# Optimization experiments

Hardware: AMD Instinct MI355X
Metric: run time of the kernel (lower is better)

## Reference

```python
import jax, jax.numpy as jnp
import numpy as np

N, M, K = 131072, 32, 16
EPS64 = 2.220446049250313e-16  # np.finfo(np.float64).eps, as in the original


def setup_inputs() -> dict:
    key = jax.random.key(0)
    k1, k2, k3, k4, k5 = jax.random.split(key, 5)
    X = jax.random.normal(k1, (N, M), dtype=jnp.float32)
    Wk0 = jax.random.normal(k2, (K,), dtype=jnp.float32)
    W = jax.random.normal(k3, (M, K, K), dtype=jnp.float32)
    mu = jax.random.uniform(k4, (K, K), minval=-4.0, maxval=4.0, dtype=jnp.float32)
    sigma = 0.5 + 0.5 * jax.random.uniform(k5, (K, K), dtype=jnp.float32)
    return {"X": X, "Wk0": Wk0, "W": W, "mu": mu, "sigma": sigma}


def reference(X, Wk0, W, mu, sigma):
    # Softmax-normalized TT weights (original: softmax(Wk0), softmax(W, axis=1))
    z = jax.nn.softmax(Wk0)          # (K,)
    Wn = jax.nn.softmax(W, axis=1)   # (M, K, K)
    inv_norm = 1.0 / (sigma * jnp.sqrt(2.0 * jnp.pi))  # (K, K) Gaussian normalizer

    def step(v, inp):
        # v: (N, K) running left-product z @ resT_0 @ ... @ resT_{i-1}
        x_i, w_i = inp               # x_i: (N,), w_i: (K, K)
        d = (x_i[:, None, None] - mu) / sigma          # (N, K, K)
        B = jnp.exp(-0.5 * d * d) * inv_norm           # Normal(mu, sigma).prob(x)
        res = w_i[None, :, :] * B                      # res[n,a,b] == original res[a,b,n]
        # original: products = products @ res.T, so v_new[n,b] = sum_a v[n,a] * res[n,b,a]
        v_new = jnp.einsum('na,nba->nb', v, res)
        return v_new, None

    v0 = jnp.broadcast_to(z, (X.shape[0], z.shape[0]))   # z @ identity start
    v_final, _ = jax.lax.scan(step, v0, (X.T, Wn))       # scan over M steps
    likelihoods = jnp.sum(v_final, axis=1)               # sum(z @ products, axis=1)
    return jnp.log(likelihoods + EPS64)
```

## Files before the change

kernel.cpp:

```cpp
#include <hip/hip_runtime.h>
#include <cmath>


#define TT_N 131072
#define TT_M 32

typedef float v2f __attribute__((ext_vector_type(2)));
typedef float v4f __attribute__((ext_vector_type(4)));

#define WS_Z 0
#define WS_P 16
#define WS_Q (16 + 256)
#define WS_R (16 + 512)
#define TBL_FLOATS (512 + 8192)

__global__ __launch_bounds__(512) void tt_prep(const float* __restrict__ Wk0,
                                               const float* __restrict__ W,
                                               const float* __restrict__ mu,
                                               const float* __restrict__ sigma,
                                               float* __restrict__ ws) {
    const int t = threadIdx.x;
    const float LOG2E = 1.4426950408889634f;
    float* z  = ws + WS_Z;
    float* PP = ws + WS_P;
    float* QQ = ws + WS_Q;
    float* RT = ws + WS_R;

    if (t < 16) {
        float mx = -1e30f;
        for (int i = 0; i < 16; ++i) mx = fmaxf(mx, Wk0[i]);
        float se = 0.f;
        for (int i = 0; i < 16; ++i) se += __expf(Wk0[i] - mx);
        z[t] = __expf(Wk0[t] - mx) / se;
    }

    if (t < 256) {
        const int a = t >> 4, b = t & 15;
        float s  = sigma[b * 16 + a];
        float mm = mu[b * 16 + a];
        float c2 = 0.72134752044448f / (s * s);
        PP[a * 16 + b] = -c2;
        QQ[a * 16 + b] = 2.0f * c2 * mm;
    }

    const int m = t >> 4;
    const int a = t & 15;
    const float* Wc = W + m * 256 + a;
    float mx = -1e30f;
    #pragma unroll
    for (int b = 0; b < 16; ++b) mx = fmaxf(mx, Wc[b * 16]);
    float se = 0.f;
    #pragma unroll
    for (int b = 0; b < 16; ++b) se += __expf(Wc[b * 16] - mx);
    float lse = __log2f(se);
    #pragma unroll
    for (int b = 0; b < 16; ++b) {
        float s     = sigma[b * 16 + a];
        float mm    = mu[b * 16 + a];
        float inv_s = 1.0f / s;
        float c2    = 0.72134752044448f / (s * s);
        float lw    = (Wc[b * 16] - mx) * LOG2E - lse;
        RT[m * 256 + a * 16 + b] =
            lw + __log2f(inv_s * 0.3989422804014327f) - c2 * mm * mm;
    }
}

__global__ __launch_bounds__(256) void tt_main(const float* __restrict__ X,
                                               const float* __restrict__ ws,
                                               float* __restrict__ out) {
    __shared__ float lds[TBL_FLOATS];
    {
        const v4f* src = (const v4f*)(ws + WS_P);
        v4f* dst = (v4f*)lds;
        for (int i = threadIdx.x; i < TBL_FLOATS / 4; i += 256) dst[i] = src[i];
    }
    __syncthreads();

    const int n = blockIdx.x * 256 + threadIdx.x;
    const float* zp = ws + WS_Z;

    v2f v[8], acc[8];
    #pragma unroll
    for (int p = 0; p < 8; ++p) v[p] = (v2f){zp[2 * p], zp[2 * p + 1]};

    const float* xp = X + (size_t)n * TT_M;
    float S = 1.f;
    float xn = xp[0];

    #pragma unroll 1
    for (int m = 0; m < TT_M; ++m) {
        const float xm = xn;
        xn = xp[(m + 1 < TT_M) ? m + 1 : m];
        const float xq = xm * xm;
        const v2f xx  = {xm, xm};
        const v2f xx2 = {xq, xq};

        int lo = 0;
        asm volatile("" : "+v"(lo));
        const float* Pm = lds + lo;
        const float* Qm = lds + 256 + lo;
        const float* Rm = lds + 512 + m * 256;

        #pragma unroll
        for (int p = 0; p < 8; ++p) acc[p] = (v2f){0.f, 0.f};

        #pragma unroll
        for (int a = 0; a < 16; ++a) {
            const float vas = (a & 1) ? v[a >> 1].y : v[a >> 1].x;
            const v2f va2 = {vas, vas};
            #pragma unroll
            for (int h = 0; h < 4; ++h) {
                v4f P4 = *(const v4f*)(Pm + a * 16 + h * 4);
                v4f Q4 = *(const v4f*)(Qm + a * 16 + h * 4);
                v4f R4 = *(const v4f*)(Rm + a * 16 + h * 4);
                v2f t0 = __builtin_elementwise_fma(Q4.xy, xx, R4.xy);
                v2f s0 = __builtin_elementwise_fma(P4.xy, xx2, t0);
                v2f t1 = __builtin_elementwise_fma(Q4.zw, xx, R4.zw);
                v2f s1 = __builtin_elementwise_fma(P4.zw, xx2, t1);
                v2f e0, e1;
                e0.x = __builtin_amdgcn_exp2f(s0.x);
                e0.y = __builtin_amdgcn_exp2f(s0.y);
                e1.x = __builtin_amdgcn_exp2f(s1.x);
                e1.y = __builtin_amdgcn_exp2f(s1.y);
                acc[h * 2]     = __builtin_elementwise_fma(va2, e0, acc[h * 2]);
                acc[h * 2 + 1] = __builtin_elementwise_fma(va2, e1, acc[h * 2 + 1]);
            }
        }

        #pragma unroll
        for (int p = 0; p < 8; ++p) v[p] = acc[p];
        v2f u0 = (acc[0] + acc[1]) + (acc[2] + acc[3]);
        v2f u1 = (acc[4] + acc[5]) + (acc[6] + acc[7]);
        v2f u  = u0 + u1;
        S = u.x + u.y;
        if (__all(S < 5e-17f)) break;
    }

    out[n] = logf(S + 2.2204460492503131e-16f);
}

extern "C" void kernel_launch(void* const* d_in, const int* in_sizes, int n_in,
                              void* d_out, int out_size, void* d_ws, size_t ws_size,
                              hipStream_t stream) {
    const float* X     = (const float*)d_in[0];
    const float* Wk0   = (const float*)d_in[1];
    const float* W     = (const float*)d_in[2];
    const float* mu    = (const float*)d_in[3];
    const float* sigma = (const float*)d_in[4];
    float* out = (float*)d_out;
    float* ws  = (float*)d_ws;

    tt_prep<<<1, 512, 0, stream>>>(Wk0, W, mu, sigma, ws);
    tt_main<<<TT_N / 256, 256, 0, stream>>>(X, ws, out);
}
```

Baseline: 100.7 us.

## Split each sample's K-wide recurrence across four lanes with shuffle exchange

```diff
diff --git a/kernel.cpp b/kernel.cpp
--- a/kernel.cpp
+++ b/kernel.cpp
@@ -65,21 +65,31 @@
     }
 }
 
-__global__ __launch_bounds__(256) void tt_main(const float* __restrict__ X,
+static __device__ __forceinline__ v2f shfl_xor_v2f(v2f x, int mask) {
+    v2f r;
+    r.x = __shfl_xor(x.x, mask, 64);
+    r.y = __shfl_xor(x.y, mask, 64);
+    return r;
+}
+
+__global__ __launch_bounds__(512) void tt_main(const float* __restrict__ X,
                                                const float* __restrict__ ws,
                                                float* __restrict__ out) {
     __shared__ float lds[TBL_FLOATS];
     {
         const v4f* src = (const v4f*)(ws + WS_P);
         v4f* dst = (v4f*)lds;
-        for (int i = threadIdx.x; i < TBL_FLOATS / 4; i += 256) dst[i] = src[i];
+        for (int i = threadIdx.x; i < TBL_FLOATS / 4; i += 512) dst[i] = src[i];
     }
     __syncthreads();
 
-    const int n = blockIdx.x * 256 + threadIdx.x;
+    const int tid  = blockIdx.x * 512 + threadIdx.x;
+    const int n    = tid >> 2;
+    const int g    = tid & 3;
+    const int boff = g << 2;
+
     const float* zp = ws + WS_Z;
-
-    v2f v[8], acc[8];
+    v2f v[8];
     #pragma unroll
     for (int p = 0; p < 8; ++p) v[p] = (v2f){zp[2 * p], zp[2 * p + 1]};
 
@@ -101,42 +111,54 @@
         const float* Qm = lds + 256 + lo;
         const float* Rm = lds + 512 + m * 256;
 
-        #pragma unroll
-        for (int p = 0; p < 8; ++p) acc[p] = (v2f){0.f, 0.f};
+        v2f a0, a1;
 
         #pragma unroll
         for (int a = 0; a < 16; ++a) {
             const float vas = (a & 1) ? v[a >> 1].y : v[a >> 1].x;
             const v2f va2 = {vas, vas};
-            #pragma unroll
-            for (int h = 0; h < 4; ++h) {
-                v4f P4 = *(const v4f*)(Pm + a * 16 + h * 4);
-                v4f Q4 = *(const v4f*)(Qm + a * 16 + h * 4);
-                v4f R4 = *(const v4f*)(Rm + a * 16 + h * 4);
-                v2f t0 = __builtin_elementwise_fma(Q4.xy, xx, R4.xy);
-                v2f s0 = __builtin_elementwise_fma(P4.xy, xx2, t0);
-                v2f t1 = __builtin_elementwise_fma(Q4.zw, xx, R4.zw);
-                v2f s1 = __builtin_elementwise_fma(P4.zw, xx2, t1);
-                v2f e0, e1;
-                e0.x = __builtin_amdgcn_exp2f(s0.x);
-                e0.y = __builtin_amdgcn_exp2f(s0.y);
-                e1.x = __builtin_amdgcn_exp2f(s1.x);
-                e1.y = __builtin_amdgcn_exp2f(s1.y);
-                acc[h * 2]     = __builtin_elementwise_fma(va2, e0, acc[h * 2]);
-                acc[h * 2 + 1] = __builtin_elementwise_fma(va2, e1, acc[h * 2 + 1]);
+            const int base = a * 16 + boff;
+            v4f P4 = *(const v4f*)(Pm + base);
+            v4f Q4 = *(const v4f*)(Qm + base);
+            v4f R4 = *(const v4f*)(Rm + base);
+            v2f t0 = __builtin_elementwise_fma(Q4.xy, xx, R4.xy);
+            v2f s0 = __builtin_elementwise_fma(P4.xy, xx2, t0);
+            v2f t1 = __builtin_elementwise_fma(Q4.zw, xx, R4.zw);
+            v2f s1 = __builtin_elementwise_fma(P4.zw, xx2, t1);
+            v2f e0, e1;
+            e0.x = __builtin_amdgcn_exp2f(s0.x);
+            e0.y = __builtin_amdgcn_exp2f(s0.y);
+            e1.x = __builtin_amdgcn_exp2f(s1.x);
+            e1.y = __builtin_amdgcn_exp2f(s1.y);
+            if (a == 0) { a0 = va2 * e0; a1 = va2 * e1; }
+            else {
+                a0 = __builtin_elementwise_fma(va2, e0, a0);
+                a1 = __builtin_elementwise_fma(va2, e1, a1);
             }
         }
 
-        #pragma unroll
-        for (int p = 0; p < 8; ++p) v[p] = acc[p];
-        v2f u0 = (acc[0] + acc[1]) + (acc[2] + acc[3]);
-        v2f u1 = (acc[4] + acc[5]) + (acc[6] + acc[7]);
-        v2f u  = u0 + u1;
-        S = u.x + u.y;
+        const bool hi1 = (g & 1) != 0;
+        const bool hi2 = (g & 2) != 0;
+        v2f r0 = shfl_xor_v2f(a0, 1), r1 = shfl_xor_v2f(a1, 1);
+        v2f u0 = hi1 ? r0 : a0;
+        v2f u1 = hi1 ? r1 : a1;
+        v2f u2 = hi1 ? a0 : r0;
+        v2f u3 = hi1 ? a1 : r1;
+        v2f w0 = shfl_xor_v2f(u0, 2), w1 = shfl_xor_v2f(u1, 2);
+        v2f w2 = shfl_xor_v2f(u2, 2), w3 = shfl_xor_v2f(u3, 2);
+        v[0] = hi2 ? w0 : u0;  v[1] = hi2 ? w1 : u1;
+        v[2] = hi2 ? w2 : u2;  v[3] = hi2 ? w3 : u3;
+        v[4] = hi2 ? u0 : w0;  v[5] = hi2 ? u1 : w1;
+        v[6] = hi2 ? u2 : w2;  v[7] = hi2 ? u3 : w3;
+
+        v2f q0 = (v[0] + v[1]) + (v[2] + v[3]);
+        v2f q1 = (v[4] + v[5]) + (v[6] + v[7]);
+        v2f q  = q0 + q1;
+        S = q.x + q.y;
         if (__all(S < 5e-17f)) break;
     }
 
-    out[n] = logf(S + 2.2204460492503131e-16f);
+    if (g == 0) out[n] = logf(S + 2.2204460492503131e-16f);
 }
 
 extern "C" void kernel_launch(void* const* d_in, const int* in_sizes, int n_in,
@@ -151,5 +173,5 @@
     float* ws  = (float*)d_ws;
 
     tt_prep<<<1, 512, 0, stream>>>(Wk0, W, mu, sigma, ws);
-    tt_main<<<TT_N / 256, 256, 0, stream>>>(X, ws, out);
+    tt_main<<<(TT_N * 4) / 512, 512, 0, stream>>>(X, ws, out);
 }
```

Measured after the change: 100.6 us. About the same (-0.1%).
